# Optimization experiments

Hardware: AMD Instinct MI355X
Metric: run time of the kernel (lower is better)

## Reference

```python
import jax, jax.numpy as jnp
import numpy as np

N = 8192
D_IN = 1024
D_OUT = 1024


def setup_inputs() -> dict:
    key = jax.random.key(0)
    ks = jax.random.split(key, 7)
    s = 1.0 / np.sqrt(D_IN)
    return {
        "feat": jax.random.normal(ks[0], (N, D_IN), dtype=jnp.float32),
        "Wq": jax.random.uniform(ks[1], (D_IN, D_OUT), jnp.float32, -s, s),
        "bq": jax.random.uniform(ks[2], (D_OUT,), jnp.float32, -s, s),
        "Wk": jax.random.uniform(ks[3], (D_IN, D_OUT), jnp.float32, -s, s),
        "bk": jax.random.uniform(ks[4], (D_OUT,), jnp.float32, -s, s),
        "Wv": jax.random.uniform(ks[5], (D_IN, D_OUT), jnp.float32, -s, s),
        "bv": jax.random.uniform(ks[6], (D_OUT,), jnp.float32, -s, s),
    }


def reference(feat, Wq, bq, Wk, bk, Wv, bv):
    # eval mode: dropout(p=0.3, training=False) is identity
    q = feat @ Wq + bq          # [N, D_OUT]
    k = feat @ Wk + bk          # [N, D_OUT]
    v = feat @ Wv + bv          # [N, D_OUT]
    scale = 1.0 / jnp.sqrt(jnp.float32(D_OUT))
    scores = (q @ k.T) * scale  # [N, N]
    attn = jax.nn.softmax(scores, axis=1)
    return attn @ v             # [N, D_OUT]
```

## Files before the change

### kernel.cpp

```cpp
#include <hip/hip_runtime.h>
#include <hip/hip_bf16.h>
#include <stdint.h>

typedef __hip_bfloat16 bf16;
typedef __attribute__((ext_vector_type(8))) short short8;
typedef __attribute__((ext_vector_type(4))) float f32x4;

#define BM 128
#define BN 128

__device__ __forceinline__ unsigned short f2bf_bits(float x) {
    return __builtin_bit_cast(unsigned short, __float2bfloat16(x));
}

__device__ __forceinline__ void gload_lds16(const bf16* g, bf16* l) {
    __builtin_amdgcn_global_load_lds(
        (const __attribute__((address_space(1))) void*)(const void*)g,
        (__attribute__((address_space(3))) void*)(void*)l,
        16, 0, 0);
}

template <int N>
__device__ __forceinline__ void waitvm() {
    if constexpr (N == 0) asm volatile("s_waitcnt vmcnt(0)" ::: "memory");
    else if constexpr (N == 3) asm volatile("s_waitcnt vmcnt(3)" ::: "memory");
    else if constexpr (N == 4) asm volatile("s_waitcnt vmcnt(4)" ::: "memory");
    else if constexpr (N == 6) asm volatile("s_waitcnt vmcnt(6)" ::: "memory");
    else if constexpr (N == 8) asm volatile("s_waitcnt vmcnt(8)" ::: "memory");
}

__global__ void prep_kernel(const float* __restrict__ feat, unsigned short* __restrict__ featb,
                            const float* __restrict__ W0, const float* __restrict__ W1,
                            const float* __restrict__ W2, bf16* __restrict__ Wt,
                            float* __restrict__ lsum) {
    const int b = blockIdx.x;
    const int tid = threadIdx.x;
    if (b < 8192) {
        int i = b * 256 + tid;
        float4 v = reinterpret_cast<const float4*>(feat)[i];
        ushort4 o;
        o.x = f2bf_bits(v.x); o.y = f2bf_bits(v.y);
        o.z = f2bf_bits(v.z); o.w = f2bf_bits(v.w);
        reinterpret_cast<ushort4*>(featb)[i] = o;
    } else if (b < 11264) {
        __shared__ float tile[32][33];
        const int b2 = b - 8192;
        const int z = b2 >> 10;
        const int t = b2 & 1023;
        const int bx = t & 31, by = t >> 5;
        const int tx = tid & 31, ty = tid >> 5;
        const float* in = (z == 0) ? W0 : (z == 1) ? W1 : W2;
        bf16* out = Wt + (size_t)z * 1024 * 1024;
        for (int r = ty; r < 32; r += 8)
            tile[r][tx] = in[(size_t)(by * 32 + r) * 1024 + bx * 32 + tx];
        __syncthreads();
        for (int r = ty; r < 32; r += 8)
            out[(size_t)(bx * 32 + r) * 1024 + by * 32 + tx] = __float2bfloat16(tile[tx][r]);
    } else {
        for (int i = tid; i < 8192; i += 256) lsum[i] = 0.f;
    }
}

__global__ void scale_rows(float* __restrict__ out, const float* __restrict__ lsum) {
    int i = blockIdx.x * 256 + threadIdx.x;
    float4 v = reinterpret_cast<float4*>(out)[i];
    float inv = 1.0f / lsum[i >> 8];
    v.x *= inv; v.y *= inv; v.z *= inv; v.w *= inv;
    reinterpret_cast<float4*>(out)[i] = v;
}

template <int MODE, int KH, int SWAP>
__global__ __launch_bounds__(256, 4)
void gemm_bt(const bf16* __restrict__ A, const bf16* __restrict__ B,
             const float* __restrict__ b0, const float* __restrict__ b1,
             const float* __restrict__ b2, float* __restrict__ lsum,
             bf16* __restrict__ outb, float* __restrict__ outf,
             int M, int N, int K, int ldb, int ldout, float scale) {
    constexpr int TILE = 128 * 32;
    constexpr int SELEMS = (2 * KH * TILE < 9216) ? 9216 : 2 * KH * TILE;
    __shared__ bf16 smem[SELEMS];
    bf16* As = smem;
    bf16* Bs = smem + KH * TILE;

    const int tid  = threadIdx.x;
    const int lane = tid & 63;
    const int wave = tid >> 6;
    const int wm = wave & 1, wn = wave >> 1;
    const int l16  = lane & 15;
    const int quad = lane >> 4;
    long bm0, bn0;
    if (SWAP == 2) {
        const int lin = blockIdx.y * 8 + blockIdx.x;
        const int xcd = lin & 7;
        const int s   = lin >> 3;
        bn0 = (long)(s & 7) * BN;
        bm0 = (long)((s >> 3) * 8 + xcd) * BM;
    } else {
        bm0 = (long)(SWAP ? blockIdx.y : blockIdx.x) * BM;
        bn0 = (long)(SWAP ? blockIdx.x : blockIdx.y) * BN;
    }

    const bf16* Ause = A;
    const bf16* Buse = B;
    bf16* oz = outb;
    int  ldo = ldout;
    int  z   = 0;
    if (MODE == 0) {
        z = blockIdx.z;
        if (z == 2) {
            bm0  = (long)blockIdx.y * BM;
            bn0  = (long)blockIdx.x * BN;
            Ause = B + (size_t)2 * N * K;
            Buse = A;
            oz   = outb + (size_t)2 * M * ldout;
            ldo  = M;
        } else {
            Buse = B + (size_t)z * N * K;
            oz   = outb + (size_t)z * M * ldout;
        }
    }

    const int lrow = lane >> 2;
    const int lcol = (lane & 3) * 8;
    const bf16* gA[2][KH];
    const bf16* gB[2][KH];
    bf16* lA[2][KH];
    bf16* lB[2][KH];
#pragma unroll
    for (int u = 0; u < 2; u++)
#pragma unroll
        for (int h = 0; h < KH; h++) {
            gA[u][h] = Ause + (size_t)(bm0 + wave * 32 + u * 16 + lrow) * K + h * 32 + lcol;
            gB[u][h] = Buse + (size_t)(bn0 + wave * 32 + u * 16 + lrow) * ldb + h * 32 + lcol;
            lA[u][h] = As + h * TILE + (wave * 32 + u * 16) * 32;
            lB[u][h] = Bs + h * TILE + (wave * 32 + u * 16) * 32;
        }

    const bf16* Ard = As + (wm * 64 + l16) * 32 + quad * 8;
    const bf16* Brd = Bs + (wn * 64 + l16) * 32 + quad * 8;

    f32x4 acc[4][4];
    const f32x4 zero = {0.f, 0.f, 0.f, 0.f};
#pragma unroll
    for (int i = 0; i < 4; i++)
#pragma unroll
        for (int j = 0; j < 4; j++) acc[i][j] = zero;

    for (int k0 = 0; k0 < K; k0 += KH * 32) {
        __syncthreads();
#pragma unroll
        for (int u = 0; u < 2; u++)
#pragma unroll
            for (int h = 0; h < KH; h++) {
                gload_lds16(gA[u][h] + k0, lA[u][h]);
                gload_lds16(gB[u][h] + k0, lB[u][h]);
            }
        __syncthreads();
#pragma unroll
        for (int h = 0; h < KH; h++) {
            short8 af[4], bfr[4];
#pragma unroll
            for (int mi = 0; mi < 4; mi++)
                af[mi] = *reinterpret_cast<const short8*>(Ard + h * TILE + mi * 16 * 32);
#pragma unroll
            for (int ni = 0; ni < 4; ni++)
                bfr[ni] = *reinterpret_cast<const short8*>(Brd + h * TILE + ni * 16 * 32);
#pragma unroll
            for (int mi = 0; mi < 4; mi++)
#pragma unroll
                for (int ni = 0; ni < 4; ni++)
                    acc[mi][ni] = __builtin_amdgcn_mfma_f32_16x16x32_bf16(af[mi], bfr[ni], acc[mi][ni], 0, 0, 0);
        }
    }

    if (MODE == 0 || MODE == 1) {
        __syncthreads();
        float bcol[4];
        if (MODE == 0 && z < 2) {
            const float* bias = (z == 0) ? b0 : b1;
#pragma unroll
            for (int ni = 0; ni < 4; ni++) bcol[ni] = bias[bn0 + wn * 64 + l16 + ni * 16];
        }
#pragma unroll
        for (int mi = 0; mi < 4; mi++) {
            bf16* eb = smem + ((wave << 1) | (mi & 1)) * 1152;
#pragma unroll
            for (int r = 0; r < 4; r++) {
                float s = 0.f;
                float brow = 0.f;
                if (MODE == 0 && z == 2) brow = b2[bm0 + wm * 64 + mi * 16 + quad * 4 + r];
#pragma unroll
                for (int ni = 0; ni < 4; ni++) {
                    float v = acc[mi][ni][r];
                    if (MODE == 0) v += (z == 2) ? brow : bcol[ni];
                    else { v = __expf(v * scale); s += v; }
                    eb[(quad * 4 + r) * 72 + ni * 16 + l16] = __float2bfloat16(v);
                }
                if (MODE == 1) {
                    s += __shfl_xor(s, 1);
                    s += __shfl_xor(s, 2);
                    s += __shfl_xor(s, 4);
                    s += __shfl_xor(s, 8);
                    if (l16 == 0) atomicAdd(&lsum[bm0 + wm * 64 + mi * 16 + quad * 4 + r], s);
                }
            }
            asm volatile("s_waitcnt lgkmcnt(0)" ::: "memory");
#pragma unroll
            for (int p = 0; p < 2; p++) {
                int r2 = p * 8 + (lane >> 3);
                int c2 = (lane & 7) * 8;
                short8 val = *reinterpret_cast<const short8*>(eb + r2 * 72 + c2);
                *reinterpret_cast<short8*>(
                    oz + (size_t)(bm0 + wm * 64 + mi * 16 + r2) * ldo + bn0 + wn * 64 + c2) = val;
            }
        }
    } else {
        const int rb2 = wm * 64 + quad * 4;
        const int cb2 = wn * 64 + l16;
#pragma unroll
        for (int mi = 0; mi < 4; mi++)
#pragma unroll
            for (int r = 0; r < 4; r++) {
                long row = bm0 + rb2 + mi * 16 + r;
                float mul = (MODE == 3) ? 1.0f / lsum[row] : 0.f;
#pragma unroll
                for (int ni = 0; ni < 4; ni++) {
                    long col = bn0 + cb2 + ni * 16;
                    if (MODE == 3) outf[row * ldout + col] = acc[mi][ni][r] * mul;
                    else           outf[row * ldout + col] += acc[mi][ni][r];
                }
            }
    }
}

__global__ __launch_bounds__(256, 2)
void gemm2b_qk(const bf16* __restrict__ A, const bf16* __restrict__ B,
               float* __restrict__ lsum, bf16* __restrict__ outb,
               int M, int N, int K, int ldb, int ldout, float scale) {
    constexpr int TA = 256 * 32;
    constexpr int SB = TA + 128 * 32;
    __shared__ __align__(16) bf16 smem[2 * SB];

    const int tid  = threadIdx.x;
    const int lane = tid & 63;
    const int wave = tid >> 6;
    const int wm   = wave >> 1;
    const int wn   = wave & 1;
    const int l16  = lane & 15;
    const int quad = lane >> 4;
    const int lrow = lane >> 2;
    const int lcol = (lane & 3) * 8;

    const long bm0 = (long)blockIdx.x * 256;
    const long bn0 = (long)blockIdx.y * 128;

    const bf16* gA[4];
    const bf16* gB[2];
    int lA[4], lB[2];
#pragma unroll
    for (int j = 0; j < 4; j++) {
        gA[j] = A + (size_t)(bm0 + j * 64 + wave * 16 + lrow) * K + lcol;
        lA[j] = (j * 64 + wave * 16) * 32;
    }
#pragma unroll
    for (int j = 0; j < 2; j++) {
        gB[j] = B + (size_t)(bn0 + j * 64 + wave * 16 + lrow) * ldb + lcol;
        lB[j] = TA + (j * 64 + wave * 16) * 32;
    }

    const int ardo = (wm * 128 + l16) * 32 + quad * 8;
    const int brdo = TA + (wn * 64 + l16) * 32 + quad * 8;
    const int T = K / 32;

    f32x4 acc[8][4];
    const f32x4 zero = {0.f, 0.f, 0.f, 0.f};
#pragma unroll
    for (int i = 0; i < 8; i++)
#pragma unroll
        for (int j = 0; j < 4; j++) acc[i][j] = zero;

    auto stageA = [&](int u) {
        bf16* sl = smem + (size_t)(u & 1) * SB;
        size_t ko = (size_t)u * 32;
#pragma unroll
        for (int j = 0; j < 4; j++) gload_lds16(gA[j] + ko, sl + lA[j]);
    };
    auto stageB = [&](int u) {
        bf16* sl = smem + (size_t)(u & 1) * SB;
        size_t ko = (size_t)u * 32;
#pragma unroll
        for (int j = 0; j < 2; j++) gload_lds16(gB[j] + ko, sl + lB[j]);
    };

    stageA(0); stageB(0);
    stageA(1); stageB(1);
    waitvm<6>();
    __builtin_amdgcn_s_barrier();

    for (int t = 0; t < T; ++t) {
        const bf16* sl = smem + (size_t)(t & 1) * SB;
        short8 bfr[4];
#pragma unroll
        for (int jp = 0; jp < 2; ++jp) {
            short8 af[4];
            if (jp == 0) {
#pragma unroll
                for (int n = 0; n < 4; n++)
                    bfr[n] = *reinterpret_cast<const short8*>(sl + brdo + n * 512);
            }
#pragma unroll
            for (int m = 0; m < 4; m++)
                af[m] = *reinterpret_cast<const short8*>(sl + ardo + (jp * 4 + m) * 512);
            __builtin_amdgcn_s_barrier();
            asm volatile("s_waitcnt lgkmcnt(0)" ::: "memory");
            __builtin_amdgcn_sched_barrier(0);
            __builtin_amdgcn_s_setprio(1);
#pragma unroll
            for (int m = 0; m < 4; m++)
#pragma unroll
                for (int n = 0; n < 4; n++)
                    acc[jp * 4 + m][n] = __builtin_amdgcn_mfma_f32_16x16x32_bf16(
                        af[m], bfr[n], acc[jp * 4 + m][n], 0, 0, 0);
            __builtin_amdgcn_s_setprio(0);
            __builtin_amdgcn_s_barrier();
            if (t + 2 < T) {
                if (jp == 0) stageB(t + 2);
                else         stageA(t + 2);
            }
        }
        if (t + 1 < T) {
            if (t + 2 < T) waitvm<6>();
            else           waitvm<0>();
            __builtin_amdgcn_s_barrier();
        }
    }
    __syncthreads();

#pragma unroll
    for (int mi = 0; mi < 8; mi++) {
        bf16* eb = smem + ((wave << 1) | (mi & 1)) * 1152;
#pragma unroll
        for (int r = 0; r < 4; r++) {
            float s = 0.f;
#pragma unroll
            for (int ni = 0; ni < 4; ni++) {
                float v = __expf(acc[mi][ni][r] * scale);
                s += v;
                eb[(quad * 4 + r) * 72 + ni * 16 + l16] = __float2bfloat16(v);
            }
            s += __shfl_xor(s, 1);
            s += __shfl_xor(s, 2);
            s += __shfl_xor(s, 4);
            s += __shfl_xor(s, 8);
            if (l16 == 0)
                atomicAdd(&lsum[bm0 + wm * 128 + mi * 16 + quad * 4 + r], s);
        }
        asm volatile("s_waitcnt lgkmcnt(0)" ::: "memory");
#pragma unroll
        for (int p = 0; p < 2; p++) {
            int r2 = p * 8 + (lane >> 3);
            int c2 = (lane & 7) * 8;
            short8 val = *reinterpret_cast<const short8*>(eb + r2 * 72 + c2);
            *reinterpret_cast<short8*>(
                outb + (size_t)(bm0 + wm * 128 + mi * 16 + r2) * ldout + bn0 + wn * 64 + c2) = val;
        }
    }
}

extern "C" void kernel_launch(void* const* d_in, const int* in_sizes, int n_in,
                              void* d_out, int out_size, void* d_ws, size_t ws_size,
                              hipStream_t stream) {
    const float* feat = (const float*)d_in[0];
    const float* Wq   = (const float*)d_in[1];
    const float* bqv  = (const float*)d_in[2];
    const float* Wk   = (const float*)d_in[3];
    const float* bkv  = (const float*)d_in[4];
    const float* Wv   = (const float*)d_in[5];
    const float* bvv  = (const float*)d_in[6];
    float* outp = (float*)d_out;

    const int M = 8192, D = 1024;
    char* ws = (char*)d_ws;
    size_t off = 0;
    auto carve = [&](size_t bytes) -> char* {
        char* r = ws + off;
        off += (bytes + 255) & ~(size_t)255;
        return r;
    };
    bf16* featb = (bf16*)carve((size_t)M * D * 2);
    bf16* Wbt   = (bf16*)carve((size_t)3 * D * D * 2);
    bf16* qk    = (bf16*)carve((size_t)2 * M * D * 2 + (size_t)D * M * 2);
    bf16* vbt   = qk + (size_t)2 * M * D;
    float* lsum = (float*)carve((size_t)M * 4);
    size_t avail = (ws_size > off) ? ws_size - off : 0;

    int C;
    if      (avail >= (size_t)M * M * 2)    C = M;
    else if (avail >= (size_t)M * 4096 * 2) C = 4096;
    else if (avail >= (size_t)M * 2048 * 2) C = 2048;
    else                                    C = 1024;
    bf16* Pc = (bf16*)carve((size_t)M * C * 2);

    prep_kernel<<<dim3(11265), dim3(256), 0, stream>>>(
        feat, (unsigned short*)featb, Wq, Wk, Wv, Wbt, lsum);
    gemm_bt<0, 2, 0><<<dim3(M / 128, D / 128, 3), dim3(256), 0, stream>>>(
        featb, Wbt, bqv, bkv, bvv, nullptr, qk, nullptr, M, D, D, D, D, 1.0f);

    const float scale = 0.03125f;
    bf16* qb = qk;
    bf16* kb = qk + (size_t)M * D;
    if (C == M) {
        gemm2b_qk<<<dim3(M / 256, M / 128), dim3(256), 0, stream>>>(
            qb, kb, lsum, Pc, M, M, D, D, M, scale);
        gemm_bt<3, 2, 2><<<dim3(D / 128, M / 128), dim3(256), 0, stream>>>(
            Pc, vbt, nullptr, nullptr, nullptr, lsum, nullptr, outp, M, D, M, M, D, 0.f);
    } else {
        hipMemsetAsync(outp, 0, (size_t)M * D * 4, stream);
        for (int c = 0; c < M / C; c++) {
            gemm_bt<1, 2, 0><<<dim3(M / 128, C / 128), dim3(256), 0, stream>>>(
                qb, kb + (size_t)c * C * D, nullptr, nullptr, nullptr, lsum, Pc, nullptr,
                M, C, D, D, C, scale);
            gemm_bt<2, 2, 1><<<dim3(D / 128, M / 128), dim3(256), 0, stream>>>(
                Pc, vbt + (size_t)c * C, nullptr, nullptr, nullptr, nullptr, nullptr, outp,
                M, D, C, M, D, 0.f);
        }
        scale_rows<<<dim3(M * D / 4 / 256), dim3(256), 0, stream>>>(outp, lsum);
    }
}
```

Measured before the change: 440.1 us.

## Replace QK^T kernel with 256x256-tile 8-wave GEMM using swizzled LDS

Replaces the 256x128-tile, 4-wave QK^T score kernel with a 512-thread kernel that computes 256x256 tiles with a K-step of 64. It XOR-swizzles the LDS layout to avoid bank conflicts and remaps block IDs so neighbouring blocks share A and B rows in cache. Loads are staged per half-tile, spread across the four compute phases of each K iteration. The larger tile cuts global and LDS traffic per MFMA, but it uses one block per CU with more LDS, which lowers occupancy and raises pipeline complexity.

```diff
diff --git a/kernel.cpp b/kernel.cpp
--- a/kernel.cpp
+++ b/kernel.cpp
@@ -23,10 +23,8 @@
 template <int N>
 __device__ __forceinline__ void waitvm() {
     if constexpr (N == 0) asm volatile("s_waitcnt vmcnt(0)" ::: "memory");
-    else if constexpr (N == 3) asm volatile("s_waitcnt vmcnt(3)" ::: "memory");
     else if constexpr (N == 4) asm volatile("s_waitcnt vmcnt(4)" ::: "memory");
     else if constexpr (N == 6) asm volatile("s_waitcnt vmcnt(6)" ::: "memory");
-    else if constexpr (N == 8) asm volatile("s_waitcnt vmcnt(8)" ::: "memory");
 }
 
 __global__ void prep_kernel(const float* __restrict__ feat, unsigned short* __restrict__ featb,
@@ -233,44 +231,53 @@
     }
 }
 
-__global__ __launch_bounds__(256, 2)
-void gemm2b_qk(const bf16* __restrict__ A, const bf16* __restrict__ B,
-               float* __restrict__ lsum, bf16* __restrict__ outb,
-               int M, int N, int K, int ldb, int ldout, float scale) {
-    constexpr int TA = 256 * 32;
-    constexpr int SB = TA + 128 * 32;
-    __shared__ __align__(16) bf16 smem[2 * SB];
+__global__ __launch_bounds__(512, 1)
+void gemm8q(const bf16* __restrict__ A, const bf16* __restrict__ B,
+            float* __restrict__ lsum, bf16* __restrict__ outb,
+            int K, int ldout, float scale) {
+    __shared__ __align__(16) bf16 smem[8 * 8192];
 
     const int tid  = threadIdx.x;
     const int lane = tid & 63;
-    const int wave = tid >> 6;
-    const int wm   = wave >> 1;
-    const int wn   = wave & 1;
+    const int w    = tid >> 6;
+    const int wm   = w >> 2;
+    const int wn   = w & 3;
     const int l16  = lane & 15;
     const int quad = lane >> 4;
-    const int lrow = lane >> 2;
-    const int lcol = (lane & 3) * 8;
-
-    const long bm0 = (long)blockIdx.x * 256;
-    const long bn0 = (long)blockIdx.y * 128;
-
-    const bf16* gA[4];
-    const bf16* gB[2];
-    int lA[4], lB[2];
-#pragma unroll
-    for (int j = 0; j < 4; j++) {
-        gA[j] = A + (size_t)(bm0 + j * 64 + wave * 16 + lrow) * K + lcol;
-        lA[j] = (j * 64 + wave * 16) * 32;
-    }
-#pragma unroll
-    for (int j = 0; j < 2; j++) {
-        gB[j] = B + (size_t)(bn0 + j * 64 + wave * 16 + lrow) * ldb + lcol;
-        lB[j] = TA + (j * 64 + wave * 16) * 32;
-    }
-
-    const int ardo = (wm * 128 + l16) * 32 + quad * 8;
-    const int brdo = TA + (wn * 64 + l16) * 32 + quad * 8;
-    const int T = K / 32;
+
+    const int bid = blockIdx.x;
+    const int s   = (bid & 7) * 128 + (bid >> 3);
+    const long bm0 = (long)(s >> 5) * 256;
+    const long bn0 = (long)(s & 31) * 256;
+
+    const int srow = lane >> 3;
+    const int scol = ((lane & 7) ^ srow) * 8;
+    const bf16* gAs[2][2];
+    const bf16* gBs[2][2];
+#pragma unroll
+    for (int h = 0; h < 2; h++)
+#pragma unroll
+        for (int c = 0; c < 2; c++) {
+            gAs[h][c] = A + (size_t)(bm0 + h * 128 + c * 64 + w * 8 + srow) * K + scol;
+            gBs[h][c] = B + (size_t)(bn0 + h * 128 + c * 64 + w * 8 + srow) * K + scol;
+        }
+    auto stg = [&](const bf16* const* src, int mh, int u) {
+        bf16* base = smem + (size_t)((((u & 1) << 2) | mh) * 8192) + w * 512;
+        gload_lds16(src[0] + (size_t)u * 64, base);
+        gload_lds16(src[1] + (size_t)u * 64, base + 4096);
+    };
+
+    const int swzb = (l16 & 7) << 4;
+    int colE[2];
+#pragma unroll
+    for (int ks = 0; ks < 2; ks++)
+        colE[ks] = ((ks * 64 + quad * 16) ^ swzb) >> 1;
+    const int arow = l16;
+    const int brow = (wn & 1) * 64 + l16;
+    const int slA = (0 << 1) | wm;
+    const int slB = (1 << 1) | (wn >> 1);
+
+    const int T = K / 64;
 
     f32x4 acc[8][4];
     const f32x4 zero = {0.f, 0.f, 0.f, 0.f};
@@ -279,81 +286,80 @@
 #pragma unroll
         for (int j = 0; j < 4; j++) acc[i][j] = zero;
 
-    auto stageA = [&](int u) {
-        bf16* sl = smem + (size_t)(u & 1) * SB;
-        size_t ko = (size_t)u * 32;
-#pragma unroll
-        for (int j = 0; j < 4; j++) gload_lds16(gA[j] + ko, sl + lA[j]);
-    };
-    auto stageB = [&](int u) {
-        bf16* sl = smem + (size_t)(u & 1) * SB;
-        size_t ko = (size_t)u * 32;
-#pragma unroll
-        for (int j = 0; j < 2; j++) gload_lds16(gB[j] + ko, sl + lB[j]);
-    };
-
-    stageA(0); stageB(0);
-    stageA(1); stageB(1);
+    stg(gAs[0], 0, 0); stg(gAs[1], 1, 0); stg(gBs[0], 2, 0); stg(gBs[1], 3, 0);
+    stg(gAs[0], 0, 1); stg(gBs[0], 2, 1); stg(gBs[1], 3, 1);
     waitvm<6>();
     __builtin_amdgcn_s_barrier();
 
-    for (int t = 0; t < T; ++t) {
-        const bf16* sl = smem + (size_t)(t & 1) * SB;
-        short8 bfr[4];
-#pragma unroll
-        for (int jp = 0; jp < 2; ++jp) {
-            short8 af[4];
-            if (jp == 0) {
-#pragma unroll
-                for (int n = 0; n < 4; n++)
-                    bfr[n] = *reinterpret_cast<const short8*>(sl + brdo + n * 512);
-            }
-#pragma unroll
-            for (int m = 0; m < 4; m++)
-                af[m] = *reinterpret_cast<const short8*>(sl + ardo + (jp * 4 + m) * 512);
+    for (int u = 0; u < T; ++u) {
+        const bf16* sa = smem + (size_t)((((u & 1) << 2) | slA) * 8192);
+        const bf16* sb = smem + (size_t)((((u & 1) << 2) | slB) * 8192);
+        short8 bfr[2][4];
+#pragma unroll
+        for (int r = 0; r < 4; ++r) {
+            short8 af[2][2];
+            if (r == 0) {
+#pragma unroll
+                for (int ks = 0; ks < 2; ks++)
+#pragma unroll
+                    for (int ni = 0; ni < 4; ni++)
+                        bfr[ks][ni] = *reinterpret_cast<const short8*>(
+                            sb + (brow + ni * 16) * 64 + colE[ks]);
+            }
+#pragma unroll
+            for (int j = 0; j < 2; j++)
+#pragma unroll
+                for (int ks = 0; ks < 2; ks++)
+                    af[j][ks] = *reinterpret_cast<const short8*>(
+                        sa + ((r * 2 + j) * 16 + arow) * 64 + colE[ks]);
+            if (r == 0) asm volatile("s_waitcnt lgkmcnt(8)" ::: "memory");
             __builtin_amdgcn_s_barrier();
             asm volatile("s_waitcnt lgkmcnt(0)" ::: "memory");
             __builtin_amdgcn_sched_barrier(0);
             __builtin_amdgcn_s_setprio(1);
 #pragma unroll
-            for (int m = 0; m < 4; m++)
-#pragma unroll
-                for (int n = 0; n < 4; n++)
-                    acc[jp * 4 + m][n] = __builtin_amdgcn_mfma_f32_16x16x32_bf16(
-                        af[m], bfr[n], acc[jp * 4 + m][n], 0, 0, 0);
+            for (int j = 0; j < 2; j++)
+#pragma unroll
+                for (int ks = 0; ks < 2; ks++)
+#pragma unroll
+                    for (int ni = 0; ni < 4; ni++)
+                        acc[r * 2 + j][ni] = __builtin_amdgcn_mfma_f32_16x16x32_bf16(
+                            af[j][ks], bfr[ks][ni], acc[r * 2 + j][ni], 0, 0, 0);
             __builtin_amdgcn_s_setprio(0);
             __builtin_amdgcn_s_barrier();
-            if (t + 2 < T) {
-                if (jp == 0) stageB(t + 2);
-                else         stageA(t + 2);
-            }
-        }
-        if (t + 1 < T) {
-            if (t + 2 < T) waitvm<6>();
-            else           waitvm<0>();
-            __builtin_amdgcn_s_barrier();
+            if (r == 0) {
+                if (u + 1 < T) stg(gAs[1], 1, u + 1);
+                if (u + 2 < T) stg(gBs[0], 2, u + 2);
+            } else if (r == 1) {
+                if (u + 2 < T) stg(gBs[1], 3, u + 2);
+            } else if (r == 2) {
+                if (u + 2 < T)      waitvm<4>();
+                else if (u + 1 < T) waitvm<0>();
+            } else {
+                if (u + 2 < T) stg(gAs[0], 0, u + 2);
+            }
         }
     }
     __syncthreads();
 
 #pragma unroll
     for (int mi = 0; mi < 8; mi++) {
-        bf16* eb = smem + ((wave << 1) | (mi & 1)) * 1152;
+        bf16* eb = smem + ((w << 1) | (mi & 1)) * 1152;
 #pragma unroll
         for (int r = 0; r < 4; r++) {
-            float s = 0.f;
+            float ssum = 0.f;
 #pragma unroll
             for (int ni = 0; ni < 4; ni++) {
                 float v = __expf(acc[mi][ni][r] * scale);
-                s += v;
+                ssum += v;
                 eb[(quad * 4 + r) * 72 + ni * 16 + l16] = __float2bfloat16(v);
             }
-            s += __shfl_xor(s, 1);
-            s += __shfl_xor(s, 2);
-            s += __shfl_xor(s, 4);
-            s += __shfl_xor(s, 8);
+            ssum += __shfl_xor(ssum, 1);
+            ssum += __shfl_xor(ssum, 2);
+            ssum += __shfl_xor(ssum, 4);
+            ssum += __shfl_xor(ssum, 8);
             if (l16 == 0)
-                atomicAdd(&lsum[bm0 + wm * 128 + mi * 16 + quad * 4 + r], s);
+                atomicAdd(&lsum[bm0 + wm * 128 + mi * 16 + quad * 4 + r], ssum);
         }
         asm volatile("s_waitcnt lgkmcnt(0)" ::: "memory");
 #pragma unroll
@@ -410,8 +416,8 @@
     bf16* qb = qk;
     bf16* kb = qk + (size_t)M * D;
     if (C == M) {
-        gemm2b_qk<<<dim3(M / 256, M / 128), dim3(256), 0, stream>>>(
-            qb, kb, lsum, Pc, M, M, D, D, M, scale);
+        gemm8q<<<dim3(1024), dim3(512), 0, stream>>>(
+            qb, kb, lsum, Pc, D, M, scale);
         gemm_bt<3, 2, 2><<<dim3(D / 128, M / 128), dim3(256), 0, stream>>>(
             Pc, vbt, nullptr, nullptr, nullptr, lsum, nullptr, outp, M, D, M, M, D, 0.f);
     } else {
```

New measurement: 502.0 us. 14.1% more time.

## Replace QK and PV GEMMs with B-from-global kernel staging only A in LDS

Applied to the files above, without the earlier changes.

Replaces the specialized 256x128 QK^T kernel and the PV gemm_bt call with a new templated kernel that stages only the A tile through LDS (64-deep k-steps, double buffered) and reads B fragments directly from global memory into registers. The tile shrinks to 128x128, and the PV pass gets an XCD-aware block remapping. The goal is less LDS traffic and fewer barriers per k-step. The trade-off is uncached direct global loads of B on the MFMA critical path and the loss of the previous fine-grained vmcnt pipelining, which may expose memory latency.

```diff
diff --git a/kernel.cpp b/kernel.cpp
--- a/kernel.cpp
+++ b/kernel.cpp
@@ -18,15 +18,6 @@
         (const __attribute__((address_space(1))) void*)(const void*)g,
         (__attribute__((address_space(3))) void*)(void*)l,
         16, 0, 0);
-}
-
-template <int N>
-__device__ __forceinline__ void waitvm() {
-    if constexpr (N == 0) asm volatile("s_waitcnt vmcnt(0)" ::: "memory");
-    else if constexpr (N == 3) asm volatile("s_waitcnt vmcnt(3)" ::: "memory");
-    else if constexpr (N == 4) asm volatile("s_waitcnt vmcnt(4)" ::: "memory");
-    else if constexpr (N == 6) asm volatile("s_waitcnt vmcnt(6)" ::: "memory");
-    else if constexpr (N == 8) asm volatile("s_waitcnt vmcnt(8)" ::: "memory");
 }
 
 __global__ void prep_kernel(const float* __restrict__ feat, unsigned short* __restrict__ featb,
@@ -233,137 +224,137 @@
     }
 }
 
+template <int MODE, int SWAP>
 __global__ __launch_bounds__(256, 2)
-void gemm2b_qk(const bf16* __restrict__ A, const bf16* __restrict__ B,
-               float* __restrict__ lsum, bf16* __restrict__ outb,
-               int M, int N, int K, int ldb, int ldout, float scale) {
-    constexpr int TA = 256 * 32;
-    constexpr int SB = TA + 128 * 32;
-    __shared__ __align__(16) bf16 smem[2 * SB];
+void gemm_bg(const bf16* __restrict__ A, const bf16* __restrict__ B,
+             float* __restrict__ lsum, bf16* __restrict__ outb,
+             float* __restrict__ outf, int M, int N, int K,
+             int ldb, int ldout, float scale) {
+    constexpr int TILE = 128 * 32;
+    __shared__ bf16 smem[2 * 2 * TILE];
 
     const int tid  = threadIdx.x;
     const int lane = tid & 63;
     const int wave = tid >> 6;
-    const int wm   = wave >> 1;
-    const int wn   = wave & 1;
+    const int wm = wave & 1, wn = wave >> 1;
     const int l16  = lane & 15;
     const int quad = lane >> 4;
+    long bm0, bn0;
+    if (SWAP == 2) {
+        const int lin = blockIdx.y * 8 + blockIdx.x;
+        const int xcd = lin & 7;
+        const int s   = lin >> 3;
+        bn0 = (long)(s & 7) * BN;
+        bm0 = (long)((s >> 3) * 8 + xcd) * BM;
+    } else {
+        bm0 = (long)blockIdx.x * BM;
+        bn0 = (long)blockIdx.y * BN;
+    }
+
     const int lrow = lane >> 2;
     const int lcol = (lane & 3) * 8;
-
-    const long bm0 = (long)blockIdx.x * 256;
-    const long bn0 = (long)blockIdx.y * 128;
-
-    const bf16* gA[4];
-    const bf16* gB[2];
-    int lA[4], lB[2];
-#pragma unroll
-    for (int j = 0; j < 4; j++) {
-        gA[j] = A + (size_t)(bm0 + j * 64 + wave * 16 + lrow) * K + lcol;
-        lA[j] = (j * 64 + wave * 16) * 32;
-    }
-#pragma unroll
-    for (int j = 0; j < 2; j++) {
-        gB[j] = B + (size_t)(bn0 + j * 64 + wave * 16 + lrow) * ldb + lcol;
-        lB[j] = TA + (j * 64 + wave * 16) * 32;
-    }
-
-    const int ardo = (wm * 128 + l16) * 32 + quad * 8;
-    const int brdo = TA + (wn * 64 + l16) * 32 + quad * 8;
-    const int T = K / 32;
-
-    f32x4 acc[8][4];
+    const bf16* gA[2][2];
+    int lA[2][2];
+#pragma unroll
+    for (int u = 0; u < 2; u++)
+#pragma unroll
+        for (int h = 0; h < 2; h++) {
+            gA[u][h] = A + (size_t)(bm0 + wave * 32 + u * 16 + lrow) * K + h * 32 + lcol;
+            lA[u][h] = h * TILE + (wave * 32 + u * 16) * 32;
+        }
+
+    const int ardo = (wm * 64 + l16) * 32 + quad * 8;
+    const bf16* gBf[4];
+#pragma unroll
+    for (int ni = 0; ni < 4; ni++)
+        gBf[ni] = B + (size_t)(bn0 + wn * 64 + ni * 16 + l16) * ldb + quad * 8;
+
+    f32x4 acc[4][4];
     const f32x4 zero = {0.f, 0.f, 0.f, 0.f};
 #pragma unroll
-    for (int i = 0; i < 8; i++)
+    for (int i = 0; i < 4; i++)
 #pragma unroll
         for (int j = 0; j < 4; j++) acc[i][j] = zero;
 
-    auto stageA = [&](int u) {
-        bf16* sl = smem + (size_t)(u & 1) * SB;
-        size_t ko = (size_t)u * 32;
-#pragma unroll
-        for (int j = 0; j < 4; j++) gload_lds16(gA[j] + ko, sl + lA[j]);
+    auto stageA = [&](int buf, int k0) {
+        bf16* dst = smem + buf * 2 * TILE;
+#pragma unroll
+        for (int u = 0; u < 2; u++)
+#pragma unroll
+            for (int h = 0; h < 2; h++)
+                gload_lds16(gA[u][h] + k0, dst + lA[u][h]);
     };
-    auto stageB = [&](int u) {
-        bf16* sl = smem + (size_t)(u & 1) * SB;
-        size_t ko = (size_t)u * 32;
-#pragma unroll
-        for (int j = 0; j < 2; j++) gload_lds16(gB[j] + ko, sl + lB[j]);
-    };
-
-    stageA(0); stageB(0);
-    stageA(1); stageB(1);
-    waitvm<6>();
-    __builtin_amdgcn_s_barrier();
-
-    for (int t = 0; t < T; ++t) {
-        const bf16* sl = smem + (size_t)(t & 1) * SB;
-        short8 bfr[4];
-#pragma unroll
-        for (int jp = 0; jp < 2; ++jp) {
-            short8 af[4];
-            if (jp == 0) {
-#pragma unroll
-                for (int n = 0; n < 4; n++)
-                    bfr[n] = *reinterpret_cast<const short8*>(sl + brdo + n * 512);
-            }
-#pragma unroll
-            for (int m = 0; m < 4; m++)
-                af[m] = *reinterpret_cast<const short8*>(sl + ardo + (jp * 4 + m) * 512);
-            __builtin_amdgcn_s_barrier();
+
+    stageA(0, 0);
+    __syncthreads();
+
+    const int NS = K / 64;
+    for (int s = 0; s < NS; ++s) {
+        const int k0 = s * 64;
+        const bf16* Ard = smem + (s & 1) * 2 * TILE + ardo;
+        if (s + 1 < NS) stageA((s + 1) & 1, k0 + 64);
+#pragma unroll
+        for (int h = 0; h < 2; h++) {
+            short8 af[4], bfr[4];
+#pragma unroll
+            for (int ni = 0; ni < 4; ni++)
+                bfr[ni] = *reinterpret_cast<const short8*>(gBf[ni] + k0 + h * 32);
+#pragma unroll
+            for (int mi = 0; mi < 4; mi++)
+                af[mi] = *reinterpret_cast<const short8*>(Ard + h * TILE + mi * 16 * 32);
+#pragma unroll
+            for (int mi = 0; mi < 4; mi++)
+#pragma unroll
+                for (int ni = 0; ni < 4; ni++)
+                    acc[mi][ni] = __builtin_amdgcn_mfma_f32_16x16x32_bf16(af[mi], bfr[ni], acc[mi][ni], 0, 0, 0);
+        }
+        __syncthreads();
+    }
+
+    if constexpr (MODE == 1) {
+#pragma unroll
+        for (int mi = 0; mi < 4; mi++) {
+            bf16* eb = smem + ((wave << 1) | (mi & 1)) * 1152;
+#pragma unroll
+            for (int r = 0; r < 4; r++) {
+                float s = 0.f;
+#pragma unroll
+                for (int ni = 0; ni < 4; ni++) {
+                    float v = __expf(acc[mi][ni][r] * scale);
+                    s += v;
+                    eb[(quad * 4 + r) * 72 + ni * 16 + l16] = __float2bfloat16(v);
+                }
+                s += __shfl_xor(s, 1);
+                s += __shfl_xor(s, 2);
+                s += __shfl_xor(s, 4);
+                s += __shfl_xor(s, 8);
+                if (l16 == 0) atomicAdd(&lsum[bm0 + wm * 64 + mi * 16 + quad * 4 + r], s);
+            }
             asm volatile("s_waitcnt lgkmcnt(0)" ::: "memory");
-            __builtin_amdgcn_sched_barrier(0);
-            __builtin_amdgcn_s_setprio(1);
-#pragma unroll
-            for (int m = 0; m < 4; m++)
-#pragma unroll
-                for (int n = 0; n < 4; n++)
-                    acc[jp * 4 + m][n] = __builtin_amdgcn_mfma_f32_16x16x32_bf16(
-                        af[m], bfr[n], acc[jp * 4 + m][n], 0, 0, 0);
-            __builtin_amdgcn_s_setprio(0);
-            __builtin_amdgcn_s_barrier();
-            if (t + 2 < T) {
-                if (jp == 0) stageB(t + 2);
-                else         stageA(t + 2);
-            }
-        }
-        if (t + 1 < T) {
-            if (t + 2 < T) waitvm<6>();
-            else           waitvm<0>();
-            __builtin_amdgcn_s_barrier();
-        }
-    }
-    __syncthreads();
-
-#pragma unroll
-    for (int mi = 0; mi < 8; mi++) {
-        bf16* eb = smem + ((wave << 1) | (mi & 1)) * 1152;
-#pragma unroll
-        for (int r = 0; r < 4; r++) {
-            float s = 0.f;
-#pragma unroll
-            for (int ni = 0; ni < 4; ni++) {
-                float v = __expf(acc[mi][ni][r] * scale);
-                s += v;
-                eb[(quad * 4 + r) * 72 + ni * 16 + l16] = __float2bfloat16(v);
-            }
-            s += __shfl_xor(s, 1);
-            s += __shfl_xor(s, 2);
-            s += __shfl_xor(s, 4);
-            s += __shfl_xor(s, 8);
-            if (l16 == 0)
-                atomicAdd(&lsum[bm0 + wm * 128 + mi * 16 + quad * 4 + r], s);
-        }
-        asm volatile("s_waitcnt lgkmcnt(0)" ::: "memory");
-#pragma unroll
-        for (int p = 0; p < 2; p++) {
-            int r2 = p * 8 + (lane >> 3);
-            int c2 = (lane & 7) * 8;
-            short8 val = *reinterpret_cast<const short8*>(eb + r2 * 72 + c2);
-            *reinterpret_cast<short8*>(
-                outb + (size_t)(bm0 + wm * 128 + mi * 16 + r2) * ldout + bn0 + wn * 64 + c2) = val;
-        }
+#pragma unroll
+            for (int p = 0; p < 2; p++) {
+                int r2 = p * 8 + (lane >> 3);
+                int c2 = (lane & 7) * 8;
+                short8 val = *reinterpret_cast<const short8*>(eb + r2 * 72 + c2);
+                *reinterpret_cast<short8*>(
+                    outb + (size_t)(bm0 + wm * 64 + mi * 16 + r2) * ldout + bn0 + wn * 64 + c2) = val;
+            }
+        }
+    } else {
+        const int rb2 = wm * 64 + quad * 4;
+        const int cb2 = wn * 64 + l16;
+#pragma unroll
+        for (int mi = 0; mi < 4; mi++)
+#pragma unroll
+            for (int r = 0; r < 4; r++) {
+                long row = bm0 + rb2 + mi * 16 + r;
+                float mul = 1.0f / lsum[row];
+#pragma unroll
+                for (int ni = 0; ni < 4; ni++) {
+                    long col = bn0 + cb2 + ni * 16;
+                    outf[row * ldout + col] = acc[mi][ni][r] * mul;
+                }
+            }
     }
 }
 
@@ -410,10 +401,10 @@
     bf16* qb = qk;
     bf16* kb = qk + (size_t)M * D;
     if (C == M) {
-        gemm2b_qk<<<dim3(M / 256, M / 128), dim3(256), 0, stream>>>(
-            qb, kb, lsum, Pc, M, M, D, D, M, scale);
-        gemm_bt<3, 2, 2><<<dim3(D / 128, M / 128), dim3(256), 0, stream>>>(
-            Pc, vbt, nullptr, nullptr, nullptr, lsum, nullptr, outp, M, D, M, M, D, 0.f);
+        gemm_bg<1, 0><<<dim3(M / 128, M / 128), dim3(256), 0, stream>>>(
+            qb, kb, lsum, Pc, nullptr, M, M, D, D, M, scale);
+        gemm_bg<3, 2><<<dim3(8, M / 128), dim3(256), 0, stream>>>(
+            Pc, vbt, lsum, nullptr, outp, M, D, M, M, D, 0.f);
     } else {
         hipMemsetAsync(outp, 0, (size_t)M * D * 4, stream);
         for (int c = 0; c < M / C; c++) {
```

After: 681.7 us. 54.9% more time.
